# Optimization experiments

Measured on AMD Instinct MI355X. Metric: run time of the kernel, lower is better.

Reference implementation:

```python
import jax, jax.numpy as jnp
import numpy as np

N_QUBITS = 20
N_BLOCKS = 3
C64 = jnp.complex64


def _u3(theta, phi, lam):
    # U3(theta, phi, lam) = [[cos(t/2), -e^{i lam} sin(t/2)],
    #                        [e^{i phi} sin(t/2), e^{i(phi+lam)} cos(t/2)]]
    ct = jnp.cos(theta / 2).astype(C64)
    st = jnp.sin(theta / 2).astype(C64)
    el = jnp.exp(1j * lam.astype(C64))
    ep = jnp.exp(1j * phi.astype(C64))
    return jnp.stack([jnp.stack([ct, -el * st]),
                      jnp.stack([ep * st, ep * el * ct])])


def _cu3(theta, phi, lam):
    # controlled-U3: identity on control=|0>, U3 on control=|1>
    u = _u3(theta, phi, lam)
    m = jnp.zeros((4, 4), C64)
    m = m.at[:2, :2].set(jnp.eye(2, dtype=C64))
    m = m.at[2:, 2:].set(u)
    return m


def _apply1(psi, m, q):
    # psi: (2,)*N_QUBITS complex state tensor; apply 2x2 gate on qubit q
    psi = jnp.moveaxis(psi, q, 0).reshape(2, -1)
    psi = m @ psi
    return jnp.moveaxis(psi.reshape((2,) * N_QUBITS), 0, q)


def _apply2(psi, m4, c, t):
    # apply 4x4 gate on (control c, target t)
    psi = jnp.moveaxis(psi, (c, t), (0, 1)).reshape(4, -1)
    psi = m4 @ psi
    return jnp.moveaxis(psi.reshape((2,) * N_QUBITS), (0, 1), (c, t))


def _forward(u3_params, cu3_params):
    psi = jnp.zeros((2,) * N_QUBITS, C64).at[(0,) * N_QUBITS].set(1.0)
    for k in range(N_BLOCKS):
        for q in range(N_QUBITS):
            psi = _apply1(psi, _u3(*u3_params[k, q]), q)
        for q in range(N_QUBITS):  # circular CU3 ring: (q, (q+1) % n)
            psi = _apply2(psi, _cu3(*cu3_params[k, q]), q, (q + 1) % N_QUBITS)
    probs = (jnp.abs(psi) ** 2).reshape(2 ** N_QUBITS, 1)
    easy_scale_coeff = 2.0 ** (N_QUBITS - 1)
    gamma, beta, alpha = 0.1, 0.8, 0.3
    x = (beta * jnp.tanh(gamma * easy_scale_coeff * probs)) ** alpha
    return x - jnp.mean(x)


def setup_inputs() -> dict:
    key = jax.random.key(0)
    k1, k2 = jax.random.split(key)
    u3_params = jax.random.normal(k1, (N_BLOCKS, N_QUBITS, 3), dtype=jnp.float32)
    cu3_params = jax.random.normal(k2, (N_BLOCKS, N_QUBITS, 3), dtype=jnp.float32)
    return {"u3_params": u3_params, "cu3_params": cu3_params}


def reference(u3_params, cu3_params):
    return _forward(u3_params, cu3_params)
```

## Files before the change

kernel.cpp:

```cpp
#include <hip/hip_runtime.h>
#include <cstdint>
#include <cstddef>


#define NB 512
#define NT 256
#define PHYS(L) ((L) + 2u * ((L) >> 4))

__device__ __forceinline__ float2 cmadd2(float2 m0, float2 a0, float2 m1, float2 a1) {
  float2 r;
  r.x = m0.x * a0.x - m0.y * a0.y + m1.x * a1.x - m1.y * a1.y;
  r.y = m0.x * a0.y + m0.y * a0.x + m1.x * a1.y + m1.y * a1.x;
  return r;
}

template <int BIT>
__device__ __forceinline__ void applyU3(float2* v, const float2* m) {
  float2 m00 = m[0], m01 = m[1], m10 = m[2], m11 = m[3];
#pragma unroll
  for (int j = 0; j < 8; j++)
    if (!((j >> BIT) & 1)) {
      int j1 = j | (1 << BIT);
      float2 a0 = v[j], a1 = v[j1];
      v[j] = cmadd2(m00, a0, m01, a1);
      v[j1] = cmadd2(m10, a0, m11, a1);
    }
}

template <int C, int T>
__device__ __forceinline__ void applyCU3(float2* v, const float2* m) {
  float2 u00 = m[0], u01 = m[1], u10 = m[2], u11 = m[3];
#pragma unroll
  for (int j = 0; j < 8; j++)
    if (((j >> C) & 1) && !((j >> T) & 1)) {
      int j1 = j | (1 << T);
      float2 a0 = v[j], a1 = v[j1];
      v[j] = cmadd2(u00, a0, u01, a1);
      v[j1] = cmadd2(u10, a0, u11, a1);
    }
}

template <int U0, int U1, int U2, int C01, int C12>
__device__ __forceinline__ void phase(float2* v, const float2* MU, const float2* MC) {
  if (U0 >= 0) applyU3<0>(v, MU + 4 * (U0 < 0 ? 0 : U0));
  if (U1 >= 0) applyU3<1>(v, MU + 4 * (U1 < 0 ? 0 : U1));
  if (U2 >= 0) applyU3<2>(v, MU + 4 * (U2 < 0 ? 0 : U2));
  if (C01 >= 0) applyCU3<0, 1>(v, MC + 4 * (C01 < 0 ? 0 : C01));
  if (C12 >= 0) applyCU3<1, 2>(v, MC + 4 * (C12 < 0 ? 0 : C12));
}

__device__ __forceinline__ void rot_store(float2* lds, unsigned t, const float2* v) {
#pragma unroll
  for (int q = 0; q < 4; q++) {
    unsigned Lp = 2u * t + 512u * q;
    *(float4*)&lds[PHYS(Lp)] = make_float4(v[q].x, v[q].y, v[q + 4].x, v[q + 4].y);
  }
}

__device__ __forceinline__ void rot_load(const float2* lds, unsigned t, float2* v) {
  const float4* p = (const float4*)&lds[PHYS(8u * t)];
#pragma unroll
  for (int i = 0; i < 4; i++) {
    float4 f = p[i];
    v[2 * i] = make_float2(f.x, f.y);
    v[2 * i + 1] = make_float2(f.z, f.w);
  }
}

__device__ __forceinline__ float xval(float2 a) {
  float p = a.x * a.x + a.y * a.y;
  return powf(0.8f * tanhf(52428.8f * p), 0.3f);
}

__device__ __forceinline__ void mat_from(const float* s, float2* m) {
  float st, ct, sl, cl, sp, cp, spl, cpl;
  sincosf(0.5f * s[0], &st, &ct);
  sincosf(s[2], &sl, &cl);
  sincosf(s[1], &sp, &cp);
  sincosf(s[1] + s[2], &spl, &cpl);
  m[0] = make_float2(ct, 0.f);
  m[1] = make_float2(-cl * st, -sl * st);
  m[2] = make_float2(cp * st, sp * st);
  m[3] = make_float2(cpl * ct, spl * ct);
}

template <int TYPE, int INIT, int FINAL>
__global__ __launch_bounds__(NT) void pass_k(const float* __restrict__ u3p,
                                             const float* __restrict__ cu3p, int k,
                                             const float2* __restrict__ in,
                                             float2* __restrict__ outPsi,
                                             float* __restrict__ accum,
                                             float* __restrict__ out) {
  __shared__ float2 A[2304], B[2304];
  __shared__ float2 M[160];
  __shared__ float red[4];
  unsigned t = threadIdx.x, b = blockIdx.x;

  float2 v[8];
  if (INIT) {
#pragma unroll
    for (int j = 0; j < 8; j++) v[j] = make_float2(0.f, 0.f);
    if (b == 0 && t == 0) { v[0] = make_float2(1.f, 0.f); *accum = 0.f; }
  } else {
    const float4* in4 = (const float4*)in + ((size_t)b << 10) + 4u * t;
#pragma unroll
    for (int i = 0; i < 4; i++) {
      float4 f = in4[i];
      v[2 * i] = make_float2(f.x, f.y);
      v[2 * i + 1] = make_float2(f.z, f.w);
    }
  }

  if (t < 20) mat_from(u3p + (k * 20 + t) * 3, M + 4 * t);
  else if (t >= 64 && t < 84) mat_from(cu3p + (k * 20 + (t - 64)) * 3, M + 80 + 4 * (t - 64));
  __syncthreads();

  const float2* MU = M;
  const float2* MC = M + 80;
  if (TYPE == 0) phase<0, 1, 2, 0, 1>(v, MU, MC);      else phase<-1, 11, 12, 10, 11>(v, MU, MC);
  rot_store(A, t, v); __syncthreads(); rot_load(A, t, v);
  if (TYPE == 0) phase<-1, 3, 4, 2, 3>(v, MU, MC);     else phase<-1, 13, 14, 12, 13>(v, MU, MC);
  rot_store(B, t, v); __syncthreads(); rot_load(B, t, v);
  if (TYPE == 0) phase<-1, 5, 6, 4, 5>(v, MU, MC);     else phase<-1, 15, 16, 14, 15>(v, MU, MC);
  rot_store(A, t, v); __syncthreads(); rot_load(A, t, v);
  if (TYPE == 0) phase<-1, 7, 8, 6, 7>(v, MU, MC);     else phase<-1, 17, 18, 16, 17>(v, MU, MC);
  rot_store(B, t, v); __syncthreads(); rot_load(B, t, v);
  if (TYPE == 0) phase<-1, 9, 10, 8, 9>(v, MU, MC);    else phase<-1, 19, -1, 18, 19>(v, MU, MC);

  if (!FINAL) {
    float4* o4 = (float4*)outPsi;
    unsigned base = b + ((t & 1u) << 9) + ((t >> 1) << 10);
    o4[base] = make_float4(v[0].x, v[0].y, v[4].x, v[4].y);
    o4[base + (1u << 17)] = make_float4(v[1].x, v[1].y, v[5].x, v[5].y);
    o4[base + (1u << 18)] = make_float4(v[2].x, v[2].y, v[6].x, v[6].y);
    o4[base + (3u << 17)] = make_float4(v[3].x, v[3].y, v[7].x, v[7].y);
  } else {
    float xv[8];
    float s = 0.f;
#pragma unroll
    for (int m = 0; m < 8; m++) { xv[m] = xval(v[m]); s += xv[m]; }
    float4* o4 = (float4*)out;
    unsigned base = (__brev(t) >> 24) + ((__brev(b) >> 23) << 8);
    o4[base] = make_float4(xv[0], xv[2], xv[1], xv[3]);
    o4[base + (1u << 17)] = make_float4(xv[4], xv[6], xv[5], xv[7]);
#pragma unroll
    for (int o = 32; o > 0; o >>= 1) s += __shfl_down(s, o);
    if ((t & 63u) == 0) red[t >> 6] = s;
    __syncthreads();
    if (t == 0) atomicAdd(accum, red[0] + red[1] + red[2] + red[3]);
  }
}

__global__ void fin_k(float* __restrict__ out, const float* __restrict__ accum) {
  unsigned i = blockIdx.x * blockDim.x + threadIdx.x;
  float mean = *accum * (1.f / 1048576.f);
  float4* o4 = (float4*)out;
  float4 x = o4[i];
  x.x -= mean; x.y -= mean; x.z -= mean; x.w -= mean;
  o4[i] = x;
}

extern "C" void kernel_launch(void* const* d_in, const int* in_sizes, int n_in,
                              void* d_out, int out_size, void* d_ws, size_t ws_size,
                              hipStream_t stream) {
  const float* u3p = (const float*)d_in[0];
  const float* cu3p = (const float*)d_in[1];
  float* out = (float*)d_out;

  char* ws = (char*)d_ws;
  float2* psiA = (float2*)ws;
  float2* psiB = (float2*)(ws + (size_t)8 * 1024 * 1024);
  float* accum = (float*)(ws + (size_t)16 * 1024 * 1024);

  pass_k<0, 1, 0><<<NB, NT, 0, stream>>>(u3p, cu3p, 0, nullptr, psiB, accum, out);
  pass_k<1, 0, 0><<<NB, NT, 0, stream>>>(u3p, cu3p, 0, psiB, psiA, accum, out);
  pass_k<0, 0, 0><<<NB, NT, 0, stream>>>(u3p, cu3p, 1, psiA, psiB, accum, out);
  pass_k<1, 0, 0><<<NB, NT, 0, stream>>>(u3p, cu3p, 1, psiB, psiA, accum, out);
  pass_k<0, 0, 0><<<NB, NT, 0, stream>>>(u3p, cu3p, 2, psiA, psiB, accum, out);
  pass_k<1, 0, 1><<<NB, NT, 0, stream>>>(u3p, cu3p, 2, psiB, nullptr, accum, out);
  fin_k<<<1024, 256, 0, stream>>>(out, accum);
}
```

Measured before the change: 135.8 us.

## Fuse mean subtraction into final pass via grid-wide atomic counter barrier

Removes the separate fin_k kernel. The final pass now has each block add its partial sum and then bump an atomic counter. Each block spins until all 512 blocks have arrived, then subtracts the mean before writing the output. This saves a kernel launch and a full read-modify-write of the 4 MB output, but it relies on all 512 blocks being co-resident, which is why __launch_bounds__(NT,2) is added. That residency assumption carries a deadlock risk, and the spin-wait has its own cost.

```diff
diff --git a/kernel.cpp b/kernel.cpp
--- a/kernel.cpp
+++ b/kernel.cpp
@@ -85,12 +85,12 @@
 }
 
 template <int TYPE, int INIT, int FINAL>
-__global__ __launch_bounds__(NT) void pass_k(const float* __restrict__ u3p,
-                                             const float* __restrict__ cu3p, int k,
-                                             const float2* __restrict__ in,
-                                             float2* __restrict__ outPsi,
-                                             float* __restrict__ accum,
-                                             float* __restrict__ out) {
+__global__ __launch_bounds__(NT, 2) void pass_k(const float* __restrict__ u3p,
+                                                const float* __restrict__ cu3p, int k,
+                                                const float2* __restrict__ in,
+                                                float2* __restrict__ outPsi,
+                                                float* __restrict__ accum,
+                                                float* __restrict__ out) {
   __shared__ float2 A[2304], B[2304];
   __shared__ float2 M[160];
   __shared__ float red[4];
@@ -100,7 +100,11 @@
   if (INIT) {
 #pragma unroll
     for (int j = 0; j < 8; j++) v[j] = make_float2(0.f, 0.f);
-    if (b == 0 && t == 0) { v[0] = make_float2(1.f, 0.f); *accum = 0.f; }
+    if (b == 0 && t == 0) {
+      v[0] = make_float2(1.f, 0.f);
+      accum[0] = 0.f;
+      *(unsigned*)(accum + 1) = 0u;
+    }
   } else {
     const float4* in4 = (const float4*)in + ((size_t)b << 10) + 4u * t;
 #pragma unroll
@@ -139,25 +143,33 @@
     float s = 0.f;
 #pragma unroll
     for (int m = 0; m < 8; m++) { xv[m] = xval(v[m]); s += xv[m]; }
-    float4* o4 = (float4*)out;
-    unsigned base = (__brev(t) >> 24) + ((__brev(b) >> 23) << 8);
-    o4[base] = make_float4(xv[0], xv[2], xv[1], xv[3]);
-    o4[base + (1u << 17)] = make_float4(xv[4], xv[6], xv[5], xv[7]);
 #pragma unroll
     for (int o = 32; o > 0; o >>= 1) s += __shfl_down(s, o);
     if ((t & 63u) == 0) red[t >> 6] = s;
     __syncthreads();
-    if (t == 0) atomicAdd(accum, red[0] + red[1] + red[2] + red[3]);
+    if (t == 0) {
+      unsigned* cnt = (unsigned*)(accum + 1);
+      float tot = red[0] + red[1] + red[2] + red[3];
+      float oldv = __hip_atomic_fetch_add(accum, tot, __ATOMIC_RELAXED,
+                                          __HIP_MEMORY_SCOPE_AGENT);
+      asm volatile("" ::"v"(oldv));
+      asm volatile("s_waitcnt vmcnt(0)" ::: "memory");
+      __hip_atomic_fetch_add(cnt, 1u, __ATOMIC_RELAXED, __HIP_MEMORY_SCOPE_AGENT);
+      unsigned c;
+      do {
+        __builtin_amdgcn_s_sleep(8);
+        c = __hip_atomic_load(cnt, __ATOMIC_RELAXED, __HIP_MEMORY_SCOPE_AGENT);
+      } while (c < NB);
+      red[0] = __hip_atomic_load(accum, __ATOMIC_RELAXED, __HIP_MEMORY_SCOPE_AGENT);
+    }
+    __syncthreads();
+    float mean = red[0] * (1.f / 1048576.f);
+    float4* o4 = (float4*)out;
+    unsigned base = (__brev(t) >> 24) + ((__brev(b) >> 23) << 8);
+    o4[base] = make_float4(xv[0] - mean, xv[2] - mean, xv[1] - mean, xv[3] - mean);
+    o4[base + (1u << 17)] =
+        make_float4(xv[4] - mean, xv[6] - mean, xv[5] - mean, xv[7] - mean);
   }
-}
-
-__global__ void fin_k(float* __restrict__ out, const float* __restrict__ accum) {
-  unsigned i = blockIdx.x * blockDim.x + threadIdx.x;
-  float mean = *accum * (1.f / 1048576.f);
-  float4* o4 = (float4*)out;
-  float4 x = o4[i];
-  x.x -= mean; x.y -= mean; x.z -= mean; x.w -= mean;
-  o4[i] = x;
 }
 
 extern "C" void kernel_launch(void* const* d_in, const int* in_sizes, int n_in,
@@ -178,5 +190,4 @@
   pass_k<1, 0, 0><<<NB, NT, 0, stream>>>(u3p, cu3p, 1, psiB, psiA, accum, out);
   pass_k<0, 0, 0><<<NB, NT, 0, stream>>>(u3p, cu3p, 2, psiA, psiB, accum, out);
   pass_k<1, 0, 1><<<NB, NT, 0, stream>>>(u3p, cu3p, 2, psiB, nullptr, accum, out);
-  fin_k<<<1024, 256, 0, stream>>>(out, accum);
 }
```

Result: slower. 152.4 us (+12.2%).

## Replace LDS transposes with cross-lane swizzle gates and a single LDS exchange

Applied to the files above, without the earlier changes.

Gates on qubits that map to wavefront lane bits are now applied with ds_swizzle/shfl_xor partner exchanges instead of four LDS store/sync/load rotations. Only one LDS transpose with an XOR swizzle remains, cutting block barriers from four to one and halving shared memory use. The cost is more cross-lane ops and duplicated arithmetic, since each lane computes its own half of every 2x2 gate product. The gate ordering and index mapping must match exactly to stay correct.

```diff
diff --git a/kernel.cpp b/kernel.cpp
--- a/kernel.cpp
+++ b/kernel.cpp
@@ -5,13 +5,24 @@
 
 #define NB 512
 #define NT 256
-#define PHYS(L) ((L) + 2u * ((L) >> 4))
 
 __device__ __forceinline__ float2 cmadd2(float2 m0, float2 a0, float2 m1, float2 a1) {
   float2 r;
   r.x = m0.x * a0.x - m0.y * a0.y + m1.x * a1.x - m1.y * a1.y;
   r.y = m0.x * a0.y + m0.y * a0.x + m1.x * a1.y + m1.y * a1.x;
   return r;
+}
+
+template <int MASK>
+__device__ __forceinline__ float2 lanexor(float2 a) {
+  if constexpr (MASK == 32) {
+    return make_float2(__shfl_xor(a.x, 32), __shfl_xor(a.y, 32));
+  } else {
+    constexpr int pat = (MASK << 10) | 0x1F;
+    return make_float2(
+        __int_as_float(__builtin_amdgcn_ds_swizzle(__float_as_int(a.x), pat)),
+        __int_as_float(__builtin_amdgcn_ds_swizzle(__float_as_int(a.y), pat)));
+  }
 }
 
 template <int BIT>
@@ -40,30 +51,43 @@
     }
 }
 
-template <int U0, int U1, int U2, int C01, int C12>
-__device__ __forceinline__ void phase(float2* v, const float2* MU, const float2* MC) {
-  if (U0 >= 0) applyU3<0>(v, MU + 4 * (U0 < 0 ? 0 : U0));
-  if (U1 >= 0) applyU3<1>(v, MU + 4 * (U1 < 0 ? 0 : U1));
-  if (U2 >= 0) applyU3<2>(v, MU + 4 * (U2 < 0 ? 0 : U2));
-  if (C01 >= 0) applyCU3<0, 1>(v, MC + 4 * (C01 < 0 ? 0 : C01));
-  if (C12 >= 0) applyCU3<1, 2>(v, MC + 4 * (C12 < 0 ? 0 : C12));
-}
-
-__device__ __forceinline__ void rot_store(float2* lds, unsigned t, const float2* v) {
-#pragma unroll
-  for (int q = 0; q < 4; q++) {
-    unsigned Lp = 2u * t + 512u * q;
-    *(float4*)&lds[PHYS(Lp)] = make_float4(v[q].x, v[q].y, v[q + 4].x, v[q + 4].y);
-  }
-}
-
-__device__ __forceinline__ void rot_load(const float2* lds, unsigned t, float2* v) {
-  const float4* p = (const float4*)&lds[PHYS(8u * t)];
-#pragma unroll
-  for (int i = 0; i < 4; i++) {
-    float4 f = p[i];
-    v[2 * i] = make_float2(f.x, f.y);
-    v[2 * i + 1] = make_float2(f.z, f.w);
+template <int MASK>
+__device__ __forceinline__ void applyU3L(float2* v, const float2* m, unsigned lane) {
+  bool hi = (lane & MASK) != 0;
+  float2 s0 = hi ? m[3] : m[0];
+  float2 s1 = hi ? m[2] : m[1];
+#pragma unroll
+  for (int j = 0; j < 8; j++) {
+    float2 p = lanexor<MASK>(v[j]);
+    v[j] = cmadd2(s0, v[j], s1, p);
+  }
+}
+
+template <int C, int MASK>
+__device__ __forceinline__ void applyCU3WL(float2* v, const float2* m, unsigned lane) {
+  bool hi = (lane & MASK) != 0;
+  float2 s0 = hi ? m[3] : m[0];
+  float2 s1 = hi ? m[2] : m[1];
+#pragma unroll
+  for (int j = 0; j < 8; j++)
+    if ((j >> C) & 1) {
+      float2 p = lanexor<MASK>(v[j]);
+      v[j] = cmadd2(s0, v[j], s1, p);
+    }
+}
+
+template <int CMASK, int TMASK>
+__device__ __forceinline__ void applyCU3LL(float2* v, const float2* m, unsigned lane) {
+  bool act = (lane & CMASK) != 0;
+  bool hi = (lane & TMASK) != 0;
+  float2 s0 = hi ? m[3] : m[0];
+  float2 s1 = hi ? m[2] : m[1];
+#pragma unroll
+  for (int j = 0; j < 8; j++) {
+    float2 p = lanexor<TMASK>(v[j]);
+    float2 nv = cmadd2(s0, v[j], s1, p);
+    v[j].x = act ? nv.x : v[j].x;
+    v[j].y = act ? nv.y : v[j].y;
   }
 }
 
@@ -91,10 +115,11 @@
                                              float2* __restrict__ outPsi,
                                              float* __restrict__ accum,
                                              float* __restrict__ out) {
-  __shared__ float2 A[2304], B[2304];
+  __shared__ float2 A[2048];
   __shared__ float2 M[160];
   __shared__ float red[4];
   unsigned t = threadIdx.x, b = blockIdx.x;
+  unsigned lane = t & 63u;
 
   float2 v[8];
   if (INIT) {
@@ -117,15 +142,46 @@
 
   const float2* MU = M;
   const float2* MC = M + 80;
-  if (TYPE == 0) phase<0, 1, 2, 0, 1>(v, MU, MC);      else phase<-1, 11, 12, 10, 11>(v, MU, MC);
-  rot_store(A, t, v); __syncthreads(); rot_load(A, t, v);
-  if (TYPE == 0) phase<-1, 3, 4, 2, 3>(v, MU, MC);     else phase<-1, 13, 14, 12, 13>(v, MU, MC);
-  rot_store(B, t, v); __syncthreads(); rot_load(B, t, v);
-  if (TYPE == 0) phase<-1, 5, 6, 4, 5>(v, MU, MC);     else phase<-1, 15, 16, 14, 15>(v, MU, MC);
-  rot_store(A, t, v); __syncthreads(); rot_load(A, t, v);
-  if (TYPE == 0) phase<-1, 7, 8, 6, 7>(v, MU, MC);     else phase<-1, 17, 18, 16, 17>(v, MU, MC);
-  rot_store(B, t, v); __syncthreads(); rot_load(B, t, v);
-  if (TYPE == 0) phase<-1, 9, 10, 8, 9>(v, MU, MC);    else phase<-1, 19, -1, 18, 19>(v, MU, MC);
+  constexpr int UB = TYPE ? 11 : 1;
+  constexpr int CB = TYPE ? 10 : 0;
+
+  if (TYPE == 0) applyU3<0>(v, MU + 0);
+  applyU3<1>(v, MU + 4 * UB);
+  applyCU3<0, 1>(v, MC + 4 * CB);
+  applyU3<2>(v, MU + 4 * (UB + 1));
+  applyCU3<1, 2>(v, MC + 4 * (CB + 1));
+  applyU3L<1>(v, MU + 4 * (UB + 2), lane);
+  applyCU3WL<2, 1>(v, MC + 4 * (CB + 2), lane);
+  applyU3L<2>(v, MU + 4 * (UB + 3), lane);
+  applyCU3LL<1, 2>(v, MC + 4 * (CB + 3), lane);
+  applyU3L<4>(v, MU + 4 * (UB + 4), lane);
+  applyCU3LL<2, 4>(v, MC + 4 * (CB + 4), lane);
+  applyU3L<8>(v, MU + 4 * (UB + 5), lane);
+  applyCU3LL<4, 8>(v, MC + 4 * (CB + 5), lane);
+  applyU3L<16>(v, MU + 4 * (UB + 6), lane);
+  applyCU3LL<8, 16>(v, MC + 4 * (CB + 6), lane);
+  applyU3L<32>(v, MU + 4 * (UB + 7), lane);
+  applyCU3LL<16, 32>(v, MC + 4 * (CB + 7), lane);
+
+  {
+    unsigned baseS = (t >> 5) + 64u * (t & 31u);
+#pragma unroll
+    for (int j = 0; j < 8; j++) {
+      unsigned Lp = baseS + 8u * j;
+      A[Lp ^ ((Lp >> 6) & 15u)] = v[j];
+    }
+    __syncthreads();
+#pragma unroll
+    for (int j = 0; j < 8; j++) {
+      unsigned Lr = 8u * t + j;
+      v[j] = A[Lr ^ ((Lr >> 6) & 15u)];
+    }
+  }
+
+  applyU3<1>(v, MU + 4 * (TYPE ? 19 : 9));
+  applyCU3<0, 1>(v, MC + 4 * (TYPE ? 18 : 8));
+  if (TYPE == 0) applyU3<2>(v, MU + 4 * 10);
+  applyCU3<1, 2>(v, MC + 4 * (TYPE ? 19 : 9));
 
   if (!FINAL) {
     float4* o4 = (float4*)outPsi;
```

Result: slower. 147.9 us (+8.9%).

## Halve per-thread amplitudes, fuse CU3 with next U3, use XOR-swizzled LDS rotations

Applied to the files above, without the earlier changes.

Each block now runs 512 threads holding 4 amplitudes each instead of 256 threads holding 8. The CU3 gate is pre-multiplied with the following qubit's U3 into per-branch 2x2 matrices, so each phase applies one fused 2-qubit update. The LDS rotation becomes nine single-bit rotations per pass using an XOR swizzle instead of padding, with explicit occupancy bounds. This cuts per-thread register pressure and gate arithmetic and raises parallelism, at the cost of more LDS round trips and barriers per pass (nine instead of four).

```diff
diff --git a/kernel.cpp b/kernel.cpp
--- a/kernel.cpp
+++ b/kernel.cpp
@@ -4,8 +4,8 @@
 
 
 #define NB 512
-#define NT 256
-#define PHYS(L) ((L) + 2u * ((L) >> 4))
+#define NT 512
+#define SW(i) ((i) ^ (((i) >> 3) & 1u))
 
 __device__ __forceinline__ float2 cmadd2(float2 m0, float2 a0, float2 m1, float2 a1) {
   float2 r;
@@ -13,58 +13,29 @@
   r.y = m0.x * a0.y + m0.y * a0.x + m1.x * a1.y + m1.y * a1.x;
   return r;
 }
-
-template <int BIT>
-__device__ __forceinline__ void applyU3(float2* v, const float2* m) {
-  float2 m00 = m[0], m01 = m[1], m10 = m[2], m11 = m[3];
-#pragma unroll
-  for (int j = 0; j < 8; j++)
-    if (!((j >> BIT) & 1)) {
-      int j1 = j | (1 << BIT);
-      float2 a0 = v[j], a1 = v[j1];
-      v[j] = cmadd2(m00, a0, m01, a1);
-      v[j1] = cmadd2(m10, a0, m11, a1);
-    }
+__device__ __forceinline__ float2 cmul(float2 a, float2 b) {
+  return make_float2(a.x * b.x - a.y * b.y, a.x * b.y + a.y * b.x);
+}
+__device__ __forceinline__ float2 cadd(float2 a, float2 b) {
+  return make_float2(a.x + b.x, a.y + b.y);
 }
 
-template <int C, int T>
-__device__ __forceinline__ void applyCU3(float2* v, const float2* m) {
-  float2 u00 = m[0], u01 = m[1], u10 = m[2], u11 = m[3];
-#pragma unroll
-  for (int j = 0; j < 8; j++)
-    if (((j >> C) & 1) && !((j >> T) & 1)) {
-      int j1 = j | (1 << T);
-      float2 a0 = v[j], a1 = v[j1];
-      v[j] = cmadd2(u00, a0, u01, a1);
-      v[j1] = cmadd2(u10, a0, u11, a1);
-    }
+__device__ __forceinline__ void applyU3b0(float2* v, const float2* m) {
+  float2 m00 = m[0], m01 = m[1], m10 = m[2], m11 = m[3];
+  float2 a0 = v[0], a1 = v[1];
+  v[0] = cmadd2(m00, a0, m01, a1); v[1] = cmadd2(m10, a0, m11, a1);
+  a0 = v[2]; a1 = v[3];
+  v[2] = cmadd2(m00, a0, m01, a1); v[3] = cmadd2(m10, a0, m11, a1);
 }
-
-template <int U0, int U1, int U2, int C01, int C12>
-__device__ __forceinline__ void phase(float2* v, const float2* MU, const float2* MC) {
-  if (U0 >= 0) applyU3<0>(v, MU + 4 * (U0 < 0 ? 0 : U0));
-  if (U1 >= 0) applyU3<1>(v, MU + 4 * (U1 < 0 ? 0 : U1));
-  if (U2 >= 0) applyU3<2>(v, MU + 4 * (U2 < 0 ? 0 : U2));
-  if (C01 >= 0) applyCU3<0, 1>(v, MC + 4 * (C01 < 0 ? 0 : C01));
-  if (C12 >= 0) applyCU3<1, 2>(v, MC + 4 * (C12 < 0 ? 0 : C12));
+__device__ __forceinline__ void applyF(float2* v, const float2* W0, const float2* W1) {
+  float2 a0 = v[0], a1 = v[2];
+  v[0] = cmadd2(W0[0], a0, W0[1], a1); v[2] = cmadd2(W0[2], a0, W0[3], a1);
+  a0 = v[1]; a1 = v[3];
+  v[1] = cmadd2(W1[0], a0, W1[1], a1); v[3] = cmadd2(W1[2], a0, W1[3], a1);
 }
-
-__device__ __forceinline__ void rot_store(float2* lds, unsigned t, const float2* v) {
-#pragma unroll
-  for (int q = 0; q < 4; q++) {
-    unsigned Lp = 2u * t + 512u * q;
-    *(float4*)&lds[PHYS(Lp)] = make_float4(v[q].x, v[q].y, v[q + 4].x, v[q + 4].y);
-  }
-}
-
-__device__ __forceinline__ void rot_load(const float2* lds, unsigned t, float2* v) {
-  const float4* p = (const float4*)&lds[PHYS(8u * t)];
-#pragma unroll
-  for (int i = 0; i < 4; i++) {
-    float4 f = p[i];
-    v[2 * i] = make_float2(f.x, f.y);
-    v[2 * i + 1] = make_float2(f.z, f.w);
-  }
+__device__ __forceinline__ void applyC(float2* v, const float2* u) {
+  float2 a0 = v[1], a1 = v[3];
+  v[1] = cmadd2(u[0], a0, u[1], a1); v[3] = cmadd2(u[2], a0, u[3], a1);
 }
 
 __device__ __forceinline__ float xval(float2 a) {
@@ -85,69 +56,92 @@
 }
 
 template <int TYPE, int INIT, int FINAL>
-__global__ __launch_bounds__(NT) void pass_k(const float* __restrict__ u3p,
-                                             const float* __restrict__ cu3p, int k,
-                                             const float2* __restrict__ in,
-                                             float2* __restrict__ outPsi,
-                                             float* __restrict__ accum,
-                                             float* __restrict__ out) {
-  __shared__ float2 A[2304], B[2304];
-  __shared__ float2 M[160];
-  __shared__ float red[4];
+__global__ __launch_bounds__(NT, 4) void pass_k(const float* __restrict__ u3p,
+                                                const float* __restrict__ cu3p, int k,
+                                                const float2* __restrict__ in,
+                                                float2* __restrict__ outPsi,
+                                                float* __restrict__ accum,
+                                                float* __restrict__ out) {
+  __shared__ float4 A4[1024], B4[1024];
+  __shared__ float2 M[168];
+  __shared__ float red[8];
   unsigned t = threadIdx.x, b = blockIdx.x;
 
-  float2 v[8];
+  float2 v[4];
   if (INIT) {
-#pragma unroll
-    for (int j = 0; j < 8; j++) v[j] = make_float2(0.f, 0.f);
+    v[0] = v[1] = v[2] = v[3] = make_float2(0.f, 0.f);
     if (b == 0 && t == 0) { v[0] = make_float2(1.f, 0.f); *accum = 0.f; }
   } else {
-    const float4* in4 = (const float4*)in + ((size_t)b << 10) + 4u * t;
-#pragma unroll
-    for (int i = 0; i < 4; i++) {
-      float4 f = in4[i];
-      v[2 * i] = make_float2(f.x, f.y);
-      v[2 * i + 1] = make_float2(f.z, f.w);
+    const float4* in4 = (const float4*)in + ((size_t)b << 10) + 2u * t;
+    float4 f0 = in4[0], f1 = in4[1];
+    v[0] = make_float2(f0.x, f0.y); v[1] = make_float2(f0.z, f0.w);
+    v[2] = make_float2(f1.x, f1.y); v[3] = make_float2(f1.z, f1.w);
+  }
+
+  float2* MU = M;
+  float2* MC = M + 80;
+  if (t < 20) {
+    mat_from(u3p + (k * 20 + t) * 3, MU + 4 * t);
+  } else if (t >= 64 && t < 84) {
+    unsigned c = t - 64;
+    float2 u[4];
+    mat_from(cu3p + (k * 20 + c) * 3, u);
+    if (c == 19) {
+      MC[76] = u[0]; MC[77] = u[1]; MC[78] = u[2]; MC[79] = u[3];
+    } else {
+      float2 ut[4];
+      mat_from(u3p + (k * 20 + c + 1) * 3, ut);
+      MC[4 * c + 0] = cadd(cmul(u[0], ut[0]), cmul(u[1], ut[2]));
+      MC[4 * c + 1] = cadd(cmul(u[0], ut[1]), cmul(u[1], ut[3]));
+      MC[4 * c + 2] = cadd(cmul(u[2], ut[0]), cmul(u[3], ut[2]));
+      MC[4 * c + 3] = cadd(cmul(u[2], ut[1]), cmul(u[3], ut[3]));
     }
   }
-
-  if (t < 20) mat_from(u3p + (k * 20 + t) * 3, M + 4 * t);
-  else if (t >= 64 && t < 84) mat_from(cu3p + (k * 20 + (t - 64)) * 3, M + 80 + 4 * (t - 64));
   __syncthreads();
 
-  const float2* MU = M;
-  const float2* MC = M + 80;
-  if (TYPE == 0) phase<0, 1, 2, 0, 1>(v, MU, MC);      else phase<-1, 11, 12, 10, 11>(v, MU, MC);
-  rot_store(A, t, v); __syncthreads(); rot_load(A, t, v);
-  if (TYPE == 0) phase<-1, 3, 4, 2, 3>(v, MU, MC);     else phase<-1, 13, 14, 12, 13>(v, MU, MC);
-  rot_store(B, t, v); __syncthreads(); rot_load(B, t, v);
-  if (TYPE == 0) phase<-1, 5, 6, 4, 5>(v, MU, MC);     else phase<-1, 15, 16, 14, 15>(v, MU, MC);
-  rot_store(A, t, v); __syncthreads(); rot_load(A, t, v);
-  if (TYPE == 0) phase<-1, 7, 8, 6, 7>(v, MU, MC);     else phase<-1, 17, 18, 16, 17>(v, MU, MC);
-  rot_store(B, t, v); __syncthreads(); rot_load(B, t, v);
-  if (TYPE == 0) phase<-1, 9, 10, 8, 9>(v, MU, MC);    else phase<-1, 19, -1, 18, 19>(v, MU, MC);
+#pragma unroll
+  for (int p = 0; p < 10; ++p) {
+    if (TYPE == 0) {
+      if (p == 0) applyU3b0(v, MU);
+      applyF(v, MU + 4 * (p + 1), MC + 4 * p);
+    } else {
+      if (p < 9) applyF(v, MU + 4 * (11 + p), MC + 4 * (10 + p));
+      else       applyC(v, MC + 4 * 19);
+    }
+    if (p < 9) {
+      float4* buf = (p & 1) ? B4 : A4;
+      buf[SW(t)]        = make_float4(v[0].x, v[0].y, v[2].x, v[2].y);
+      buf[SW(t + 512u)] = make_float4(v[1].x, v[1].y, v[3].x, v[3].y);
+      __syncthreads();
+      float4 fa = buf[SW(2u * t)], fb = buf[SW(2u * t + 1u)];
+      v[0] = make_float2(fa.x, fa.y); v[1] = make_float2(fa.z, fa.w);
+      v[2] = make_float2(fb.x, fb.y); v[3] = make_float2(fb.z, fb.w);
+    }
+  }
 
   if (!FINAL) {
     float4* o4 = (float4*)outPsi;
     unsigned base = b + ((t & 1u) << 9) + ((t >> 1) << 10);
-    o4[base] = make_float4(v[0].x, v[0].y, v[4].x, v[4].y);
-    o4[base + (1u << 17)] = make_float4(v[1].x, v[1].y, v[5].x, v[5].y);
-    o4[base + (1u << 18)] = make_float4(v[2].x, v[2].y, v[6].x, v[6].y);
-    o4[base + (3u << 17)] = make_float4(v[3].x, v[3].y, v[7].x, v[7].y);
+    o4[base]              = make_float4(v[0].x, v[0].y, v[2].x, v[2].y);
+    o4[base + (1u << 18)] = make_float4(v[1].x, v[1].y, v[3].x, v[3].y);
   } else {
-    float xv[8];
-    float s = 0.f;
-#pragma unroll
-    for (int m = 0; m < 8; m++) { xv[m] = xval(v[m]); s += xv[m]; }
-    float4* o4 = (float4*)out;
-    unsigned base = (__brev(t) >> 24) + ((__brev(b) >> 23) << 8);
-    o4[base] = make_float4(xv[0], xv[2], xv[1], xv[3]);
-    o4[base + (1u << 17)] = make_float4(xv[4], xv[6], xv[5], xv[7]);
+    float xv0 = xval(v[0]), xv1 = xval(v[1]), xv2 = xval(v[2]), xv3 = xval(v[3]);
+    float s = xv0 + xv1 + xv2 + xv3;
+    float2* o2 = (float2*)out;
+    unsigned rt = __brev(t) >> 23, rb = __brev(b) >> 23;
+    unsigned base = rt + (rb << 9);
+    o2[base] = make_float2(xv0, xv1);
+    o2[base + (1u << 18)] = make_float2(xv2, xv3);
 #pragma unroll
     for (int o = 32; o > 0; o >>= 1) s += __shfl_down(s, o);
     if ((t & 63u) == 0) red[t >> 6] = s;
     __syncthreads();
-    if (t == 0) atomicAdd(accum, red[0] + red[1] + red[2] + red[3]);
+    if (t == 0) {
+      float tot = 0.f;
+#pragma unroll
+      for (int i = 0; i < 8; i++) tot += red[i];
+      atomicAdd(accum, tot);
+    }
   }
 }
 
```

After: 135.4 us. About the same (-0.3%).
